# Optimization experiments

Hardware: AMD Instinct MI355X
Metric: run time of the kernel (lower is better)

The kernel has to match this reference:

```python
import jax, jax.numpy as jnp
import numpy as np

NUM_HEADS = 8
WIN = 7  # local_window_size
HALF = WIN // 2


def setup_inputs() -> dict:
    key = jax.random.key(0)
    k1, k2, k3 = jax.random.split(key, 3)
    B, N, C = 1, 4096, 384  # N = T*H*W with T=4, H=W=32
    x = jax.random.normal(k1, (B, N, C), dtype=jnp.float32)
    w_qkv = jax.random.normal(k2, (C, 3 * C), dtype=jnp.float32) * 0.02
    w_proj = jax.random.normal(k3, (C, C), dtype=jnp.float32) * 0.02
    b_proj = jnp.zeros((C,), dtype=jnp.float32)
    return {"x": x, "w_qkv": w_qkv, "w_proj": w_proj, "b_proj": b_proj, "H": 32, "W": 32}


def _gather_windows(t):
    H, W = t.shape[3], t.shape[4]
    tp = jnp.pad(t, ((0, 0), (0, 0), (0, 0), (HALF, HALF), (HALF, HALF), (0, 0)))
    wins = [tp[:, :, :, dy:dy + H, dx:dx + W, :] for dy in range(WIN) for dx in range(WIN)]
    return jnp.stack(wins, axis=5)


def reference(x, w_qkv, w_proj, b_proj, H, W):
    B, N, C = x.shape
    nh, hd = NUM_HEADS, C // NUM_HEADS
    T = N // (H * W)
    scale = hd ** (-0.5)

    qkv = (x @ w_qkv).reshape(B, N, 3, nh, hd)
    # (B, nh, T, H, W, hd)
    q = qkv[:, :, 0].transpose(0, 2, 1, 3).reshape(B, nh, T, H, W, hd)
    k = qkv[:, :, 1].transpose(0, 2, 1, 3).reshape(B, nh, T, H, W, hd)
    v = qkv[:, :, 2].transpose(0, 2, 1, 3).reshape(B, nh, T, H, W, hd)

    kwin = _gather_windows(k)  # (B, nh, T, H, W, 49, hd); zeros at borders (NOT masked)
    vwin = _gather_windows(v)

    scores = jnp.einsum('bnthwd,bnthwkd->bnthwk', q, kwin) * scale
    attn = jax.nn.softmax(scores, axis=-1)  # zero-padded keys give score 0 -> weight exp(0)
    out = jnp.einsum('bnthwk,bnthwkd->bnthwd', attn, vwin)

    out = out.transpose(0, 2, 3, 4, 1, 5).reshape(B, N, C)
    return out @ w_proj + b_proj
```

## Files before the change

### kernel.cpp

```cpp
#include <hip/hip_runtime.h>
#include <hip/hip_bf16.h>
#include <math.h>

#define NH 8
#define HD 48
#define C_DIM 384
#define C3 1152
#define SCALE_F 0.14433756729740643f

typedef unsigned short ushort_t;
typedef __attribute__((ext_vector_type(8))) short short8;
typedef __attribute__((ext_vector_type(4))) float f32x4;

static __device__ __forceinline__ ushort_t bf16u(float f) {
    __hip_bfloat16 b = __float2bfloat16(f);
    return *(ushort_t*)&b;
}

__global__ __launch_bounds__(256) void split_all(const float* __restrict__ x,
                                                 ushort_t* __restrict__ hi,
                                                 ushort_t* __restrict__ lo,
                                                 const float* __restrict__ wq,
                                                 ushort_t* __restrict__ qhiT,
                                                 ushort_t* __restrict__ qloT,
                                                 const float* __restrict__ wp,
                                                 ushort_t* __restrict__ phiT,
                                                 ushort_t* __restrict__ ploT)
{
    const int bidx = blockIdx.x;
    if (bidx < 1536) {
        const int i = bidx * 256 + threadIdx.x;
        const float4 v = ((const float4*)x)[i];
        const float f[4] = {v.x, v.y, v.z, v.w};
        ushort_t hb[4], lb[4];
        #pragma unroll
        for (int j = 0; j < 4; ++j) {
            __hip_bfloat16 h = __float2bfloat16(f[j]);
            __hip_bfloat16 l = __float2bfloat16(f[j] - __bfloat162float(h));
            hb[j] = *(ushort_t*)&h;
            lb[j] = *(ushort_t*)&l;
        }
        *(ushort4*)(hi + i * 4) = make_ushort4(hb[0], hb[1], hb[2], hb[3]);
        *(ushort4*)(lo + i * 4) = make_ushort4(lb[0], lb[1], lb[2], lb[3]);
    } else if (bidx < 3264) {
        const int idx = (bidx - 1536) * 256 + threadIdx.x;
        const int k = idx / C3;
        const int n = idx - k * C3;
        const float v = wq[idx];
        __hip_bfloat16 h = __float2bfloat16(v);
        __hip_bfloat16 l = __float2bfloat16(v - __bfloat162float(h));
        qhiT[n * C_DIM + k] = *(ushort_t*)&h;
        qloT[n * C_DIM + k] = *(ushort_t*)&l;
    } else {
        const int idx = (bidx - 3264) * 256 + threadIdx.x;
        const int k = idx / C_DIM;
        const int n = idx - k * C_DIM;
        const float v = wp[idx];
        __hip_bfloat16 h = __float2bfloat16(v);
        __hip_bfloat16 l = __float2bfloat16(v - __bfloat162float(h));
        phiT[n * C_DIM + k] = *(ushort_t*)&h;
        ploT[n * C_DIM + k] = *(ushort_t*)&l;
    }
}

__global__ __launch_bounds__(256) void split_wT_kernel(const float* __restrict__ w,
                                                       ushort_t* __restrict__ hiT,
                                                       ushort_t* __restrict__ loT,
                                                       int K, int N)
{
    const int idx = blockIdx.x * 256 + threadIdx.x;
    if (idx >= K * N) return;
    const int k = idx / N;
    const int n = idx - k * N;
    const float v = w[idx];
    __hip_bfloat16 h = __float2bfloat16(v);
    __hip_bfloat16 l = __float2bfloat16(v - __bfloat162float(h));
    hiT[n * K + k] = *(ushort_t*)&h;
    loT[n * K + k] = *(ushort_t*)&l;
}

__global__ __launch_bounds__(256) void gemm_mfma3(const ushort_t* __restrict__ Ah,
                                                  const ushort_t* __restrict__ Al,
                                                  const ushort_t* __restrict__ BhT,
                                                  const ushort_t* __restrict__ BlT,
                                                  const float* __restrict__ bias,
                                                  float* __restrict__ C,
                                                  int N, int K, int gn)
{
    __shared__ ushort_t sAh[128 * 40];
    __shared__ ushort_t sAl[128 * 40];
    __shared__ ushort_t sBh[64 * 40];
    __shared__ ushort_t sBl[64 * 40];

    const int tid = threadIdx.x;
    const int nwg = gridDim.x;
    const int orig = blockIdx.x;
    const int wg = (orig & 7) * (nwg >> 3) + (orig >> 3);
    const int bmi = wg / gn;
    const int bni = wg - bmi * gn;
    const int bm = bmi * 128;
    const int bn = bni * 64;

    const int rowA = tid >> 2;
    const int slotA = (tid & 3) * 8;
    const int rowB = tid >> 2;
    const int slotB = (tid & 3) * 8;

    const ushort_t* gAh0 = Ah + (size_t)(bm + rowA) * K + slotA;
    const ushort_t* gAh1 = Ah + (size_t)(bm + rowA + 64) * K + slotA;
    const ushort_t* gAl0 = Al + (size_t)(bm + rowA) * K + slotA;
    const ushort_t* gAl1 = Al + (size_t)(bm + rowA + 64) * K + slotA;
    const ushort_t* gBh  = BhT + (size_t)(bn + rowB) * K + slotB;
    const ushort_t* gBl  = BlT + (size_t)(bn + rowB) * K + slotB;

    const int lane = tid & 63;
    const int wid = tid >> 6;
    const int wm = wid >> 1;
    const int wn = wid & 1;
    const int fr = lane & 15;
    const int kb = lane >> 4;
    const int aoff = (wm * 64 + fr) * 40 + kb * 8;
    const int boff = (wn * 32 + fr) * 40 + kb * 8;

    f32x4 acc[4][2] = {};

    for (int k0 = 0; k0 < K; k0 += 32) {
        const short8 va0 = *(const short8*)(gAh0 + k0);
        const short8 va1 = *(const short8*)(gAh1 + k0);
        const short8 vl0 = *(const short8*)(gAl0 + k0);
        const short8 vl1 = *(const short8*)(gAl1 + k0);
        const short8 vb0 = *(const short8*)(gBh + k0);
        const short8 vb1 = *(const short8*)(gBl + k0);
        *(short8*)&sAh[rowA * 40 + slotA]        = va0;
        *(short8*)&sAh[(rowA + 64) * 40 + slotA] = va1;
        *(short8*)&sAl[rowA * 40 + slotA]        = vl0;
        *(short8*)&sAl[(rowA + 64) * 40 + slotA] = vl1;
        *(short8*)&sBh[rowB * 40 + slotB]        = vb0;
        *(short8*)&sBl[rowB * 40 + slotB]        = vb1;
        __syncthreads();

        short8 ah[4], al[4], bh[2], bl[2];
        #pragma unroll
        for (int m = 0; m < 4; ++m) {
            ah[m] = *(const short8*)&sAh[aoff + m * 16 * 40];
            al[m] = *(const short8*)&sAl[aoff + m * 16 * 40];
        }
        #pragma unroll
        for (int n = 0; n < 2; ++n) {
            bh[n] = *(const short8*)&sBh[boff + n * 16 * 40];
            bl[n] = *(const short8*)&sBl[boff + n * 16 * 40];
        }
        #pragma unroll
        for (int m = 0; m < 4; ++m) {
            #pragma unroll
            for (int n = 0; n < 2; ++n) {
                acc[m][n] = __builtin_amdgcn_mfma_f32_16x16x32_bf16(ah[m], bh[n], acc[m][n], 0, 0, 0);
                acc[m][n] = __builtin_amdgcn_mfma_f32_16x16x32_bf16(ah[m], bl[n], acc[m][n], 0, 0, 0);
                acc[m][n] = __builtin_amdgcn_mfma_f32_16x16x32_bf16(al[m], bh[n], acc[m][n], 0, 0, 0);
            }
        }
        __syncthreads();
    }

    #pragma unroll
    for (int n = 0; n < 2; ++n) {
        const int col = bn + wn * 32 + n * 16 + fr;
        const float bv = bias ? bias[col] : 0.f;
        #pragma unroll
        for (int m = 0; m < 4; ++m) {
            const int r0 = bm + wm * 64 + m * 16 + kb * 4;
            #pragma unroll
            for (int r = 0; r < 4; ++r) {
                C[(size_t)(r0 + r) * N + col] = acc[m][n][r] + bv;
            }
        }
    }
}

__global__ __launch_bounds__(256) void gemm64(const float* __restrict__ A,
                                              const float* __restrict__ B,
                                              const float* __restrict__ bias,
                                              float* __restrict__ C,
                                              int M, int N, int K)
{
    __shared__ float As[64][17];
    __shared__ float Bs[16][64];

    const int tid = threadIdx.x;
    const int tx = tid & 15;
    const int ty = tid >> 4;
    const int bm = blockIdx.x * 64;
    const int bn = blockIdx.y * 64;
    const int arow = tid >> 2;
    const int acol = (tid & 3) << 2;
    const int brow = tid >> 4;
    const int bcol = (tid & 15) << 2;

    float acc[4][4] = {};

    for (int k0 = 0; k0 < K; k0 += 16) {
        const float4 a4 = *(const float4*)(A + (size_t)(bm + arow) * K + k0 + acol);
        const float4 b4 = *(const float4*)(B + (size_t)(k0 + brow) * N + bn + bcol);
        As[arow][acol + 0] = a4.x; As[arow][acol + 1] = a4.y;
        As[arow][acol + 2] = a4.z; As[arow][acol + 3] = a4.w;
        *(float4*)&Bs[brow][bcol] = b4;
        __syncthreads();
        #pragma unroll
        for (int kk = 0; kk < 16; ++kk) {
            const float a0 = As[ty * 4 + 0][kk];
            const float a1 = As[ty * 4 + 1][kk];
            const float a2 = As[ty * 4 + 2][kk];
            const float a3 = As[ty * 4 + 3][kk];
            const float4 b = *(const float4*)&Bs[kk][tx * 4];
            acc[0][0] = fmaf(a0, b.x, acc[0][0]); acc[0][1] = fmaf(a0, b.y, acc[0][1]);
            acc[0][2] = fmaf(a0, b.z, acc[0][2]); acc[0][3] = fmaf(a0, b.w, acc[0][3]);
            acc[1][0] = fmaf(a1, b.x, acc[1][0]); acc[1][1] = fmaf(a1, b.y, acc[1][1]);
            acc[1][2] = fmaf(a1, b.z, acc[1][2]); acc[1][3] = fmaf(a1, b.w, acc[1][3]);
            acc[2][0] = fmaf(a2, b.x, acc[2][0]); acc[2][1] = fmaf(a2, b.y, acc[2][1]);
            acc[2][2] = fmaf(a2, b.z, acc[2][2]); acc[2][3] = fmaf(a2, b.w, acc[2][3]);
            acc[3][0] = fmaf(a3, b.x, acc[3][0]); acc[3][1] = fmaf(a3, b.y, acc[3][1]);
            acc[3][2] = fmaf(a3, b.z, acc[3][2]); acc[3][3] = fmaf(a3, b.w, acc[3][3]);
        }
        __syncthreads();
    }

    float4 bb = {0.f, 0.f, 0.f, 0.f};
    if (bias) bb = *(const float4*)(bias + bn + tx * 4);
    #pragma unroll
    for (int i = 0; i < 4; ++i) {
        float4 o;
        o.x = acc[i][0] + bb.x; o.y = acc[i][1] + bb.y;
        o.z = acc[i][2] + bb.z; o.w = acc[i][3] + bb.w;
        *(float4*)(C + (size_t)(bm + ty * 4 + i) * N + bn + tx * 4) = o;
    }
}

#define KP_SHORTS 18432
#define PROW 72
__global__ __launch_bounds__(512) void local_attn_mfma5(const float* __restrict__ qkv,
                                                        ushort_t* __restrict__ outHi,
                                                        ushort_t* __restrict__ outLo)
{
    __shared__ ushort_t sKP[KP_SHORTS];
    __shared__ ushort_t sV[13504];
    __shared__ ushort_t sQ[2048];
    __shared__ float    sS[32 * 57];

    const int tid = threadIdx.x;
    const int b = blockIdx.x;
    const int t = b >> 8, h = (b >> 3) & 31, head = b & 7;

    if (tid < 288) {
        if (tid < 256) ((unsigned int*)(sKP + 17920))[tid] = 0u;
        else           ((unsigned int*)(sV + 13440))[tid - 256] = 0u;
    }

    #pragma unroll
    for (int it = 0; it < 2; ++it) {
        const int i = tid + it * 512;
        const int q = i >> 5, d = (i & 31) * 2;
        float2 v = make_float2(0.f, 0.f);
        if (d < 48)
            v = *(const float2*)(qkv + (size_t)((t << 10) + (h << 5) + q) * C3 + head * HD + d);
        const unsigned int pk = (unsigned int)bf16u(v.x * SCALE_F) | ((unsigned int)bf16u(v.y * SCALE_F) << 16);
        *(unsigned int*)&sQ[q * 64 + (d ^ ((q & 7) << 3))] = pk;
    }
    #pragma unroll
    for (int r = 0; r < 7; ++r) {
        const int hk = h + r - 3;
        const bool rowok = (unsigned)hk < 32u;
        const size_t rk = (size_t)((t << 10) + (hk << 5)) * C3 + C_DIM + head * HD;
        for (int i = tid; i < 1280; i += 512) {
            const int slot = i >> 5, d = (i & 31) * 2;
            const int c = slot - 3;
            float2 v = make_float2(0.f, 0.f);
            if (rowok && (unsigned)c < 32u && d < 48)
                v = *(const float2*)(qkv + rk + (size_t)c * C3 + d);
            const unsigned int pk = (unsigned int)bf16u(v.x) | ((unsigned int)bf16u(v.y) << 16);
            *(unsigned int*)&sKP[(r * 40 + slot) * 64 + (d ^ ((slot & 7) << 3))] = pk;
        }
    }
    __syncthreads();

    const int wv = tid >> 6, l = tid & 63, lr = l & 15, lc = l >> 4;

    float2 vreg[7][2];
    #pragma unroll
    for (int r = 0; r < 7; ++r) {
        const int hk = h + r - 3;
        const bool rowok = (unsigned)hk < 32u;
        const size_t rv = (size_t)((t << 10) + (hk << 5)) * C3 + 2 * C_DIM + head * HD;
        #pragma unroll
        for (int it = 0; it < 2; ++it) {
            const int i = tid + it * 512;
            float2 v = make_float2(0.f, 0.f);
            if (i < 960) {
                const int slot = i / 24;
                const int d = (i - slot * 24) * 2;
                const int c = slot - 3;
                if (rowok && (unsigned)c < 32u)
                    v = *(const float2*)(qkv + rv + (size_t)c * C3 + d);
            }
            vreg[r][it] = v;
        }
    }
    {
        short8 aq[2][2];
        #pragma unroll
        for (int fm = 0; fm < 2; ++fm) {
            const int q = fm * 16 + lr;
            aq[fm][0] = *(const short8*)&sQ[q * 64 + ((lc * 8) ^ ((q & 7) << 3))];
            aq[fm][1] = *(const short8*)&sQ[q * 64 + ((lc * 8 + 32) ^ ((q & 7) << 3))];
        }
        for (int u = wv; u < 21; u += 8) {
            const int r = u / 3, fn = u - r * 3;
            const int slot = fn * 16 + lr;
            const short8 b0 = *(const short8*)&sKP[(r * 40 + slot) * 64 + ((lc * 8) ^ ((slot & 7) << 3))];
            const short8 b1 = *(const short8*)&sKP[(r * 40 + slot) * 64 + ((lc * 8 + 32) ^ ((slot & 7) << 3))];
            f32x4 acc0 = {}, acc1 = {};
            acc0 = __builtin_amdgcn_mfma_f32_16x16x32_bf16(aq[0][0], b0, acc0, 0, 0, 0);
            acc0 = __builtin_amdgcn_mfma_f32_16x16x32_bf16(aq[0][1], b1, acc0, 0, 0, 0);
            acc1 = __builtin_amdgcn_mfma_f32_16x16x32_bf16(aq[1][0], b0, acc1, 0, 0, 0);
            acc1 = __builtin_amdgcn_mfma_f32_16x16x32_bf16(aq[1][1], b1, acc1, 0, 0, 0);
            #pragma unroll
            for (int reg = 0; reg < 4; ++reg) {
                const int q0 = lc * 4 + reg;
                const int dx0 = slot - q0;
                if (dx0 >= 0 && dx0 < 7) sS[q0 * 57 + r * 7 + dx0] = acc0[reg];
                const int q1 = 16 + lc * 4 + reg;
                const int dx1 = slot - q1;
                if (dx1 >= 0 && dx1 < 7) sS[q1 * 57 + r * 7 + dx1] = acc1[reg];
            }
        }
    }
    __syncthreads();

    #pragma unroll
    for (int r = 0; r < 7; ++r) {
        #pragma unroll
        for (int it = 0; it < 2; ++it) {
            const int i = tid + it * 512;
            if (i < 960) {
                const int slot = i / 24;
                const int d = (i - slot * 24) * 2;
                sV[(r * 48 + d) * 40 + slot]     = bf16u(vreg[r][it].x);
                sV[(r * 48 + d + 1) * 40 + slot] = bf16u(vreg[r][it].y);
            }
        }
    }
    if (tid < 32) {
        const int q = tid;
        float sv[49];
        #pragma unroll
        for (int j = 0; j < 49; ++j) sv[j] = sS[q * 57 + j];
        float mx = sv[0];
        #pragma unroll
        for (int j = 1; j < 49; ++j) mx = fmaxf(mx, sv[j]);
        float sum = 0.f;
        #pragma unroll
        for (int j = 0; j < 49; ++j) { sv[j] = __expf(sv[j] - mx); sum += sv[j]; }
        const float inv = 1.f / sum;
        #pragma unroll
        for (int j = 0; j < 49; ++j) {
            const int r = j / 7, dx = j - (j / 7) * 7;
            sKP[(r * 32 + q) * PROW + q + dx] = bf16u(sv[j] * inv);
        }
    } else {
        for (int i = tid - 32; i < 7 * 32 * PROW; i += 480) {
            const int row = i / PROW;
            const int col = i - row * PROW;
            const int q = row & 31;
            if ((unsigned)(col - q) >= 7u)
                sKP[i] = 0;
        }
    }
    __syncthreads();

    if (wv < 6) {
        const int fm = (wv >= 3) ? 1 : 0;
        const int fn = wv - fm * 3;
        const int q = fm * 16 + lr;
        const int dim = fn * 16 + lr;
        f32x4 acc = {};
        #pragma unroll
        for (int r = 0; r < 7; ++r) {
            const short8 a0 = *(const short8*)&sKP[(r * 32 + q) * PROW + lc * 8];
            const short8 a1 = *(const short8*)&sKP[(r * 32 + q) * PROW + lc * 8 + 32];
            const short8 b0 = *(const short8*)&sV[(r * 48 + dim) * 40 + lc * 8];
            const short8 b1 = *(const short8*)&sV[(r * 48 + dim) * 40 + lc * 8 + 32];
            acc = __builtin_amdgcn_mfma_f32_16x16x32_bf16(a0, b0, acc, 0, 0, 0);
            acc = __builtin_amdgcn_mfma_f32_16x16x32_bf16(a1, b1, acc, 0, 0, 0);
        }
        #pragma unroll
        for (int reg = 0; reg < 4; ++reg) {
            const int qq = fm * 16 + lc * 4 + reg;
            const int n = (t << 10) | (h << 5) | qq;
            const float o = acc[reg];
            __hip_bfloat16 hb = __float2bfloat16(o);
            __hip_bfloat16 lb = __float2bfloat16(o - __bfloat162float(hb));
            const size_t ob = (size_t)n * C_DIM + head * HD + dim;
            outHi[ob] = *(ushort_t*)&hb;
            outLo[ob] = *(ushort_t*)&lb;
        }
    }
}

__global__ __launch_bounds__(256) void local_attn16(const float* __restrict__ qkv,
                                                    float* __restrict__ out)
{
    const int tid = threadIdx.x;
    const int dlane = tid & 15;
    const int gid = blockIdx.x * 16 + (tid >> 4);
    const int head = gid & 7;
    const int n = gid >> 3;
    const int t = n >> 10;
    const int h = (n >> 5) & 31;
    const int w = n & 31;
    const float scale = SCALE_F;

    const float* qp = qkv + (size_t)n * C3 + head * HD;
    const float q0 = qp[dlane];
    const float q1 = qp[dlane + 16];
    const float q2 = qp[dlane + 32];

    const size_t base_k = (size_t)(C_DIM + head * HD);
    const size_t base_v = (size_t)(2 * C_DIM + head * HD);

    float s[49];
    #pragma unroll
    for (int p = 0; p < 49; ++p) {
        const int dy = p / 7, dx = p % 7;
        const int hk = h + dy - 3;
        const int wk = w + dx - 3;
        float sc = 0.f;
        if ((unsigned)hk < 32u && (unsigned)wk < 32u) {
            const int nk = (t << 10) | (hk << 5) | wk;
            const float* kp = qkv + (size_t)nk * C3 + base_k;
            float acc = q0 * kp[dlane];
            acc = fmaf(q1, kp[dlane + 16], acc);
            acc = fmaf(q2, kp[dlane + 32], acc);
            acc += __shfl_xor(acc, 1, 16);
            acc += __shfl_xor(acc, 2, 16);
            acc += __shfl_xor(acc, 4, 16);
            acc += __shfl_xor(acc, 8, 16);
            sc = acc * scale;
        }
        s[p] = sc;
    }

    float m = s[0];
    #pragma unroll
    for (int p = 1; p < 49; ++p) m = fmaxf(m, s[p]);
    float sum = 0.f;
    #pragma unroll
    for (int p = 0; p < 49; ++p) { s[p] = __expf(s[p] - m); sum += s[p]; }
    const float inv = 1.f / sum;

    float o0 = 0.f, o1 = 0.f, o2 = 0.f;
    #pragma unroll
    for (int p = 0; p < 49; ++p) {
        const int dy = p / 7, dx = p % 7;
        const int hk = h + dy - 3;
        const int wk = w + dx - 3;
        if ((unsigned)hk < 32u && (unsigned)wk < 32u) {
            const float wgt = s[p] * inv;
            const int nk = (t << 10) | (hk << 5) | wk;
            const float* vp = qkv + (size_t)nk * C3 + base_v;
            o0 = fmaf(wgt, vp[dlane],      o0);
            o1 = fmaf(wgt, vp[dlane + 16], o1);
            o2 = fmaf(wgt, vp[dlane + 32], o2);
        }
    }

    float* op = out + (size_t)n * C_DIM + head * HD;
    op[dlane]      = o0;
    op[dlane + 16] = o1;
    op[dlane + 32] = o2;
}

extern "C" void kernel_launch(void* const* d_in, const int* in_sizes, int n_in,
                              void* d_out, int out_size, void* d_ws, size_t ws_size,
                              hipStream_t stream)
{
    const float* x      = (const float*)d_in[0];
    const float* w_qkv  = (const float*)d_in[1];
    const float* w_proj = (const float*)d_in[2];
    const float* b_proj = (const float*)d_in[3];

    const int M = 4096;
    dim3 blk(256);

    const size_t NEED = 33816576;

    unsigned char* ws = (unsigned char*)d_ws;
    float* qkv = (float*)ws;
    float* att = (float*)(ws + 18874368);

    if (ws_size >= NEED) {
        ushort_t* Ah  = (ushort_t*)(ws + 25165824);
        ushort_t* Al  = (ushort_t*)(ws + 28311552);
        ushort_t* BhT = (ushort_t*)(ws + 31457280);
        ushort_t* BlT = (ushort_t*)(ws + 32342016);
        ushort_t* PhT = (ushort_t*)(ws + 33226752);
        ushort_t* PlT = (ushort_t*)(ws + 33521664);

        split_all<<<dim3(3840), blk, 0, stream>>>(x, Ah, Al, w_qkv, BhT, BlT, w_proj, PhT, PlT);

        gemm_mfma3<<<dim3(576), blk, 0, stream>>>(Ah, Al, BhT, BlT, nullptr, qkv, C3, C_DIM, 18);

        local_attn_mfma5<<<dim3(1024), dim3(512), 0, stream>>>(qkv, Ah, Al);

        gemm_mfma3<<<dim3(192), blk, 0, stream>>>(Ah, Al, PhT, PlT, b_proj, (float*)d_out, C_DIM, C_DIM, 6);
    } else {
        gemm64<<<dim3(M / 64, C3 / 64), blk, 0, stream>>>(x, w_qkv, nullptr, qkv, M, C3, C_DIM);
        local_attn16<<<dim3(2048), blk, 0, stream>>>(qkv, att);
        gemm64<<<dim3(M / 64, C_DIM / 64), blk, 0, stream>>>(att, w_proj, b_proj, (float*)d_out, M, C_DIM, C_DIM);
    }
}
```

Measured before the change: 85.41 us.

## Split local attention into separate score/softmax and PV kernels

The fused local attention kernel becomes two launches. The first computes QK scores and softmax and writes compact bf16 probabilities to a workspace buffer. The second loads V and the probabilities, expands them into the banded P layout in shared memory, and runs the PV MFMA. This is meant to cut per-block LDS and register pressure (the V register staging is gone) so more blocks can be resident. In exchange it adds a kernel launch and a global round trip for the probabilities, and drops the overlap of V loads with the score computation.

```diff
diff --git a/kernel.cpp b/kernel.cpp
--- a/kernel.cpp
+++ b/kernel.cpp
@@ -235,14 +235,11 @@
     }
 }
 
-#define KP_SHORTS 18432
-#define PROW 72
-__global__ __launch_bounds__(512) void local_attn_mfma5(const float* __restrict__ qkv,
-                                                        ushort_t* __restrict__ outHi,
-                                                        ushort_t* __restrict__ outLo)
-{
-    __shared__ ushort_t sKP[KP_SHORTS];
-    __shared__ ushort_t sV[13504];
+#define PCROW 56
+__global__ __launch_bounds__(512) void attn_scores(const float* __restrict__ qkv,
+                                                   ushort_t* __restrict__ Pc)
+{
+    __shared__ ushort_t sK[18432];
     __shared__ ushort_t sQ[2048];
     __shared__ float    sS[32 * 57];
 
@@ -250,10 +247,7 @@
     const int b = blockIdx.x;
     const int t = b >> 8, h = (b >> 3) & 31, head = b & 7;
 
-    if (tid < 288) {
-        if (tid < 256) ((unsigned int*)(sKP + 17920))[tid] = 0u;
-        else           ((unsigned int*)(sV + 13440))[tid - 256] = 0u;
-    }
+    if (tid < 256) ((unsigned int*)(sK + 17920))[tid] = 0u;
 
     #pragma unroll
     for (int it = 0; it < 2; ++it) {
@@ -277,33 +271,13 @@
             if (rowok && (unsigned)c < 32u && d < 48)
                 v = *(const float2*)(qkv + rk + (size_t)c * C3 + d);
             const unsigned int pk = (unsigned int)bf16u(v.x) | ((unsigned int)bf16u(v.y) << 16);
-            *(unsigned int*)&sKP[(r * 40 + slot) * 64 + (d ^ ((slot & 7) << 3))] = pk;
+            *(unsigned int*)&sK[(r * 40 + slot) * 64 + (d ^ ((slot & 7) << 3))] = pk;
         }
     }
     __syncthreads();
 
     const int wv = tid >> 6, l = tid & 63, lr = l & 15, lc = l >> 4;
 
-    float2 vreg[7][2];
-    #pragma unroll
-    for (int r = 0; r < 7; ++r) {
-        const int hk = h + r - 3;
-        const bool rowok = (unsigned)hk < 32u;
-        const size_t rv = (size_t)((t << 10) + (hk << 5)) * C3 + 2 * C_DIM + head * HD;
-        #pragma unroll
-        for (int it = 0; it < 2; ++it) {
-            const int i = tid + it * 512;
-            float2 v = make_float2(0.f, 0.f);
-            if (i < 960) {
-                const int slot = i / 24;
-                const int d = (i - slot * 24) * 2;
-                const int c = slot - 3;
-                if (rowok && (unsigned)c < 32u)
-                    v = *(const float2*)(qkv + rv + (size_t)c * C3 + d);
-            }
-            vreg[r][it] = v;
-        }
-    }
     {
         short8 aq[2][2];
         #pragma unroll
@@ -315,8 +289,8 @@
         for (int u = wv; u < 21; u += 8) {
             const int r = u / 3, fn = u - r * 3;
             const int slot = fn * 16 + lr;
-            const short8 b0 = *(const short8*)&sKP[(r * 40 + slot) * 64 + ((lc * 8) ^ ((slot & 7) << 3))];
-            const short8 b1 = *(const short8*)&sKP[(r * 40 + slot) * 64 + ((lc * 8 + 32) ^ ((slot & 7) << 3))];
+            const short8 b0 = *(const short8*)&sK[(r * 40 + slot) * 64 + ((lc * 8) ^ ((slot & 7) << 3))];
+            const short8 b1 = *(const short8*)&sK[(r * 40 + slot) * 64 + ((lc * 8 + 32) ^ ((slot & 7) << 3))];
             f32x4 acc0 = {}, acc1 = {};
             acc0 = __builtin_amdgcn_mfma_f32_16x16x32_bf16(aq[0][0], b0, acc0, 0, 0, 0);
             acc0 = __builtin_amdgcn_mfma_f32_16x16x32_bf16(aq[0][1], b1, acc0, 0, 0, 0);
@@ -335,19 +309,6 @@
     }
     __syncthreads();
 
-    #pragma unroll
-    for (int r = 0; r < 7; ++r) {
-        #pragma unroll
-        for (int it = 0; it < 2; ++it) {
-            const int i = tid + it * 512;
-            if (i < 960) {
-                const int slot = i / 24;
-                const int d = (i - slot * 24) * 2;
-                sV[(r * 48 + d) * 40 + slot]     = bf16u(vreg[r][it].x);
-                sV[(r * 48 + d + 1) * 40 + slot] = bf16u(vreg[r][it].y);
-            }
-        }
-    }
     if (tid < 32) {
         const int q = tid;
         float sv[49];
@@ -360,21 +321,59 @@
         #pragma unroll
         for (int j = 0; j < 49; ++j) { sv[j] = __expf(sv[j] - mx); sum += sv[j]; }
         const float inv = 1.f / sum;
-        #pragma unroll
-        for (int j = 0; j < 49; ++j) {
-            const int r = j / 7, dx = j - (j / 7) * 7;
-            sKP[(r * 32 + q) * PROW + q + dx] = bf16u(sv[j] * inv);
-        }
-    } else {
-        for (int i = tid - 32; i < 7 * 32 * PROW; i += 480) {
-            const int row = i / PROW;
-            const int col = i - row * PROW;
-            const int q = row & 31;
-            if ((unsigned)(col - q) >= 7u)
-                sKP[i] = 0;
-        }
+        ushort_t* prow = Pc + ((size_t)b * 32 + q) * PCROW;
+        #pragma unroll
+        for (int j = 0; j < 49; ++j) prow[j] = bf16u(sv[j] * inv);
+    }
+}
+
+#define PROW 72
+__global__ __launch_bounds__(512) void attn_pv(const float* __restrict__ qkv,
+                                               const ushort_t* __restrict__ Pc,
+                                               ushort_t* __restrict__ outHi,
+                                               ushort_t* __restrict__ outLo)
+{
+    __shared__ ushort_t sP[7 * 32 * PROW];
+    __shared__ ushort_t sV[13504];
+
+    const int tid = threadIdx.x;
+    const int b = blockIdx.x;
+    const int t = b >> 8, h = (b >> 3) & 31, head = b & 7;
+
+    if (tid < 32) ((unsigned int*)(sV + 13440))[tid] = 0u;
+
+    #pragma unroll
+    for (int r = 0; r < 7; ++r) {
+        const int hk = h + r - 3;
+        const bool rowok = (unsigned)hk < 32u;
+        const size_t rv = (size_t)((t << 10) + (hk << 5)) * C3 + 2 * C_DIM + head * HD;
+        for (int i = tid; i < 960; i += 512) {
+            const int slot = i / 24;
+            const int d = (i - slot * 24) * 2;
+            const int c = slot - 3;
+            float2 v = make_float2(0.f, 0.f);
+            if (rowok && (unsigned)c < 32u)
+                v = *(const float2*)(qkv + rv + (size_t)c * C3 + d);
+            sV[(r * 48 + d) * 40 + slot]     = bf16u(v.x);
+            sV[(r * 48 + d + 1) * 40 + slot] = bf16u(v.y);
+        }
+    }
+    for (int i = tid; i < 32 * 49; i += 512) {
+        const int q = i / 49;
+        const int j = i - q * 49;
+        const int r = j / 7, dx = j - (j / 7) * 7;
+        sP[(r * 32 + q) * PROW + q + dx] = Pc[((size_t)b * 32 + q) * PCROW + j];
+    }
+    for (int i = tid; i < 7 * 32 * PROW; i += 512) {
+        const int row = i / PROW;
+        const int col = i - row * PROW;
+        const int q = row & 31;
+        if ((unsigned)(col - q) >= 7u)
+            sP[i] = 0;
     }
     __syncthreads();
+
+    const int wv = tid >> 6, l = tid & 63, lr = l & 15, lc = l >> 4;
 
     if (wv < 6) {
         const int fm = (wv >= 3) ? 1 : 0;
@@ -384,8 +383,8 @@
         f32x4 acc = {};
         #pragma unroll
         for (int r = 0; r < 7; ++r) {
-            const short8 a0 = *(const short8*)&sKP[(r * 32 + q) * PROW + lc * 8];
-            const short8 a1 = *(const short8*)&sKP[(r * 32 + q) * PROW + lc * 8 + 32];
+            const short8 a0 = *(const short8*)&sP[(r * 32 + q) * PROW + lc * 8];
+            const short8 a1 = *(const short8*)&sP[(r * 32 + q) * PROW + lc * 8 + 32];
             const short8 b0 = *(const short8*)&sV[(r * 48 + dim) * 40 + lc * 8];
             const short8 b1 = *(const short8*)&sV[(r * 48 + dim) * 40 + lc * 8 + 32];
             acc = __builtin_amdgcn_mfma_f32_16x16x32_bf16(a0, b0, acc, 0, 0, 0);
@@ -497,6 +496,7 @@
     float* att = (float*)(ws + 18874368);
 
     if (ws_size >= NEED) {
+        ushort_t* Pc  = (ushort_t*)(ws + 18874368);
         ushort_t* Ah  = (ushort_t*)(ws + 25165824);
         ushort_t* Al  = (ushort_t*)(ws + 28311552);
         ushort_t* BhT = (ushort_t*)(ws + 31457280);
@@ -508,7 +508,8 @@
 
         gemm_mfma3<<<dim3(576), blk, 0, stream>>>(Ah, Al, BhT, BlT, nullptr, qkv, C3, C_DIM, 18);
 
-        local_attn_mfma5<<<dim3(1024), dim3(512), 0, stream>>>(qkv, Ah, Al);
+        attn_scores<<<dim3(1024), dim3(512), 0, stream>>>(qkv, Pc);
+        attn_pv<<<dim3(1024), dim3(512), 0, stream>>>(qkv, Pc, Ah, Al);
 
         gemm_mfma3<<<dim3(192), blk, 0, stream>>>(Ah, Al, PhT, PlT, b_proj, (float*)d_out, C_DIM, C_DIM, 6);
     } else {
```

Measured after the change: 88.98 us. +4.2%, slower.
